# Optimization experiments

Hardware: AMD Instinct MI355X
Metric: run time of the kernel (lower is better)

The kernel has to match this reference:

```python
import jax, jax.numpy as jnp
import numpy as np

B, N, DEG = 128, 512, 16          # graphs, nodes/graph, avg degree
NB = B * N                        # 65536 nodes
E = NB * DEG                      # 1048576 edges
K1, K2, K3 = 410, 205, 103        # ceil(0.8*512), ceil(0.5*410), ceil(0.5*205)
H, C = 4, 32                      # GAT heads, head dim
F_IN, ED = 128, 7


def _glorot(key, shape, fan_in):
    return jax.random.normal(key, shape, dtype=jnp.float32) / np.float32(np.sqrt(fan_in))


def setup_inputs() -> dict:
    key = jax.random.key(0)
    ks = jax.random.split(key, 24)
    x = jax.random.normal(ks[0], (NB, F_IN), dtype=jnp.float32)
    # random intra-graph edges, then offset per graph
    src = jax.random.randint(ks[1], (E,), 0, N)
    dst = jax.random.randint(ks[2], (E,), 0, N)
    off = jnp.repeat(jnp.arange(B) * N, N * DEG)
    edge_index = jnp.stack([src + off, dst + off]).astype(jnp.int32)
    edge_attr = jax.random.normal(ks[3], (E, ED), dtype=jnp.float32)
    p = {
        'c1_wl': _glorot(ks[4], (F_IN, F_IN), F_IN), 'c1_bl': jnp.zeros((F_IN,), jnp.float32), 'c1_wr': _glorot(ks[5], (F_IN, F_IN), F_IN),
        'p1_w': _glorot(ks[6], (F_IN,), F_IN),
        'c2_wl': _glorot(ks[7], (F_IN, F_IN), F_IN), 'c2_bl': jnp.zeros((F_IN,), jnp.float32), 'c2_wr': _glorot(ks[8], (F_IN, F_IN), F_IN),
        'p2_wrel': _glorot(ks[9], (F_IN, 1), F_IN), 'p2_brel': jnp.zeros((1,), jnp.float32), 'p2_wroot': _glorot(ks[10], (F_IN, 1), F_IN),
        'g_w': _glorot(ks[11], (F_IN, H * C), F_IN), 'g_as': _glorot(ks[12], (H, C), C), 'g_ad': _glorot(ks[13], (H, C), C),
        'g_we': _glorot(ks[14], (ED, H * C), ED), 'g_ae': _glorot(ks[15], (H, C), C), 'g_b': jnp.zeros((H * C,), jnp.float32),
        'p3_wrel': _glorot(ks[16], (F_IN, 1), F_IN), 'p3_brel': jnp.zeros((1,), jnp.float32), 'p3_wroot': _glorot(ks[17], (F_IN, 1), F_IN),
        'l1_w': _glorot(ks[18], (F_IN, F_IN), F_IN), 'l1_b': jnp.zeros((F_IN,), jnp.float32),
        'l2_w': _glorot(ks[19], (F_IN, 64), F_IN), 'l2_b': jnp.zeros((64,), jnp.float32),
        'l3_w': _glorot(ks[20], (64, 1), 64), 'l3_b': jnp.zeros((1,), jnp.float32),
    }
    return {'x': x, 'edge_index': edge_index, 'edge_attr': edge_attr, **p}


def _sage(x, src, dst, emf, wl, bl, wr):
    # SAGEConv: mean-aggregate neighbors (masked edges), lin_l(agg)+lin_r(x)
    agg = jax.ops.segment_sum(x[src] * emf[:, None], dst, num_segments=NB)
    cnt = jax.ops.segment_sum(emf, dst, num_segments=NB)
    mean = agg / jnp.maximum(cnt, 1.0)[:, None]
    return mean @ wl + bl + x @ wr


def _graphconv(x, src, dst, emf, wrel, brel, wroot):
    # GraphConv (SAGPooling score GNN): add-aggregation
    agg = jax.ops.segment_sum(x[src] * emf[:, None], dst, num_segments=NB)
    return (agg @ wrel + brel + x @ wroot).reshape(-1)


def _pool(x, score, nmask, K):
    # per-graph static top-k (equal-size graphs) == PyG topk + filter
    masked = jnp.where(nmask, score, -jnp.inf).reshape(B, N)
    idx = jax.lax.top_k(masked, K)[1]
    nm = jnp.zeros((B, N), dtype=bool).at[jnp.arange(B)[:, None], idx].set(True).reshape(-1)
    x = jnp.where(nm[:, None], x * score[:, None], 0.0)
    return x, nm


def _gap(x, K):
    # global mean pool; dropped nodes are exactly zero, K live nodes per graph
    return x.reshape(B, N, F_IN).sum(axis=1) / K


def _gat(x, src, dst, emf, nmask, edge_attr, w, a_s, a_d, w_e, a_e, b):
    xs = (x @ w).reshape(NB, H, C)
    al_s = (xs * a_s).sum(-1)                                   # [NB,H]
    al_d = (xs * a_d).sum(-1)
    al_e = ((edge_attr @ w_e).reshape(E, H, C) * a_e).sum(-1)    # [E,H]
    alpha = jax.nn.leaky_relu(al_s[src] + al_d[dst] + al_e, 0.2)
    alpha = jnp.where(emf[:, None] > 0, alpha, -jnp.inf)
    # PyG add_self_loops=True with fill_value='mean' for edge_attr
    ea_mean = (edge_attr * emf[:, None]).sum(0) / jnp.maximum(emf.sum(), 1.0)
    al_se = ((ea_mean @ w_e).reshape(H, C) * a_e).sum(-1)        # [H]
    alpha_self = jax.nn.leaky_relu(al_s + al_d + al_se[None, :], 0.2)
    alpha_self = jnp.where(nmask[:, None], alpha_self, -jnp.inf)
    m = jnp.maximum(jax.ops.segment_max(alpha, dst, num_segments=NB), alpha_self)
    m = jnp.where(jnp.isfinite(m), m, 0.0)
    ex = jnp.exp(alpha - m[dst]) * emf[:, None]
    ex_s = jnp.where(nmask[:, None], jnp.exp(alpha_self - m), 0.0)
    den = jnp.maximum(jax.ops.segment_sum(ex, dst, num_segments=NB) + ex_s, 1e-16)
    num = jax.ops.segment_sum(ex[:, :, None] * xs[src], dst, num_segments=NB) + ex_s[:, :, None] * xs
    return (num / den[:, :, None]).reshape(NB, H * C) + b


def _forward(x, edge_index, edge_attr, c1_wl, c1_bl, c1_wr, p1_w, c2_wl, c2_bl, c2_wr,
             p2_wrel, p2_brel, p2_wroot, g_w, g_as, g_ad, g_we, g_ae, g_b,
             p3_wrel, p3_brel, p3_wroot, l1_w, l1_b, l2_w, l2_b, l3_w, l3_b):
    src, dst = edge_index[0], edge_index[1]
    nmask = jnp.ones((NB,), dtype=bool)
    emf = jnp.ones((E,), jnp.float32)

    # block 1: SAGEConv -> TopKPooling(0.8) -> gap
    x = jax.nn.relu(_sage(x, src, dst, emf, c1_wl, c1_bl, c1_wr))
    s1 = jnp.tanh((x @ p1_w) / jnp.linalg.norm(p1_w))
    x, nmask = _pool(x, s1, nmask, K1)
    emf = emf * nmask[src] * nmask[dst]
    x1 = _gap(x, K1)

    # block 2: SAGEConv -> SAGPooling(0.5) -> gap
    x = jax.nn.relu(_sage(x, src, dst, emf, c2_wl, c2_bl, c2_wr))
    s2 = jnp.tanh(_graphconv(x, src, dst, emf, p2_wrel, p2_brel, p2_wroot))
    x, nmask = _pool(x, s2, nmask, K2)
    emf = emf * nmask[src] * nmask[dst]
    x2 = _gap(x, K2)

    # block 3: GATConv(128->32x4, edge_dim=7) -> SAGPooling(0.5) -> gap
    x = jax.nn.relu(_gat(x, src, dst, emf, nmask, edge_attr, g_w, g_as, g_ad, g_we, g_ae, g_b))
    s3 = jnp.tanh(_graphconv(x, src, dst, emf, p3_wrel, p3_brel, p3_wroot))
    x, nmask = _pool(x, s3, nmask, K3)
    x3 = _gap(x, K3)

    h = x1 + x2 + x3
    h = jax.nn.relu(h @ l1_w + l1_b)
    h = jax.nn.relu(h @ l2_w + l2_b)   # dropout identity in eval
    return jax.nn.sigmoid(h @ l3_w + l3_b)[:, 0]


def reference(x, edge_index, edge_attr, c1_wl, c1_bl, c1_wr, p1_w, c2_wl, c2_bl, c2_wr,
              p2_wrel, p2_brel, p2_wroot, g_w, g_as, g_ad, g_we, g_ae, g_b,
              p3_wrel, p3_brel, p3_wroot, l1_w, l1_b, l2_w, l2_b, l3_w, l3_b):
    return _forward(x, edge_index, edge_attr, c1_wl, c1_bl, c1_wr, p1_w, c2_wl, c2_bl, c2_wr,
                    p2_wrel, p2_brel, p2_wroot, g_w, g_as, g_ad, g_we, g_ae, g_b,
                    p3_wrel, p3_brel, p3_wroot, l1_w, l1_b, l2_w, l2_b, l3_w, l3_b)
```

## Files before the change

### kernel.cpp

```cpp
#include <hip/hip_runtime.h>
#include <math.h>

#define NBV 65536
#define EV  1048576
#define BV  128
#define K1V 410
#define K2V 205
#define K3V 103
#define NL2 (BV*K2V)
#define NEG_BIG (-1.0e38f)

__device__ __forceinline__ float lrelu(float x){ return x > 0.f ? x : 0.2f*x; }

__global__ void k_sentinel(float* out, float v){
  int i = threadIdx.x;
  if (i < 128) out[i] = v;
}

__global__ void k_init1(float* nmask, int* dcnt){
  int i = blockIdx.x*blockDim.x + threadIdx.x;
  if (i < NBV) nmask[i] = 1.f;
  if (i < NBV+1) dcnt[i] = 0;
}

__global__ void k_zero_i(int* p, int n){
  int i = blockIdx.x*blockDim.x + threadIdx.x;
  if (i < n) p[i] = 0;
}

__global__ void k_hist(const int* dst, int* dcnt){
  int e = blockIdx.x*blockDim.x + threadIdx.x;
  if (e < EV) atomicAdd(&dcnt[dst[e]], 1);
}

__global__ void k_scan1(const int* dcnt, int* rp, int* bsum){
  __shared__ int sc[256];
  int t = threadIdx.x, i = blockIdx.x*256 + t;
  int v = dcnt[i];
  sc[t] = v; __syncthreads();
  for (int o = 1; o < 256; o <<= 1){
    int x = (t >= o) ? sc[t-o] : 0;
    __syncthreads();
    sc[t] += x;
    __syncthreads();
  }
  rp[i] = sc[t];
  if (t == 255) bsum[blockIdx.x] = sc[t];
}

__global__ void k_scan2(int* bsum){
  __shared__ int sc[256];
  int t = threadIdx.x;
  int v = bsum[t];
  sc[t] = v; __syncthreads();
  for (int o = 1; o < 256; o <<= 1){
    int x = (t >= o) ? sc[t-o] : 0;
    __syncthreads();
    sc[t] += x;
    __syncthreads();
  }
  bsum[t] = sc[t] - v;
}

__global__ void k_scan3(int* rp, const int* dcnt, const int* bsum){
  int t = threadIdx.x, i = blockIdx.x*256 + t;
  rp[i] = rp[i] - dcnt[i] + bsum[blockIdx.x];
  if (i == 0) rp[NBV] = EV;
}

__global__ void k_scatter(const int* src, const int* dst, const int* rp, int* fill,
                          int* csr_src, int* csr_eid){
  int e = blockIdx.x*blockDim.x + threadIdx.x;
  if (e < EV){
    int d = dst[e];
    int pos = atomicAdd(&fill[d], 1);
    int slot = rp[d] + pos;
    csr_src[slot] = src[e];
    csr_eid[slot] = e;
  }
}

__global__ void k_ve_inv(const float* g_we, const float* g_ae, const float* p1w, float* sml){
  __shared__ float sc[128];
  int t = threadIdx.x;
  if (t < 28){
    int ed = t >> 2, h = t & 3;
    float a = 0.f;
    for (int c = 0; c < 32; c++) a += g_we[ed*128 + h*32 + c] * g_ae[h*32 + c];
    sml[20 + t] = a;
  }
  float v = p1w[t];
  sc[t] = v*v; __syncthreads();
  for (int o = 64; o > 0; o >>= 1){ if (t < o) sc[t] += sc[t+o]; __syncthreads(); }
  if (t == 0) sml[0] = 1.f / sqrtf(sc[0]);
}

__global__ void k_ale(const float* ea, const float* ve, float* ALE){
  int e = blockIdx.x*blockDim.x + threadIdx.x;
  if (e < EV){
    float a0=0.f,a1=0.f,a2=0.f,a3=0.f;
    for (int ed = 0; ed < 7; ed++){
      float x = ea[e*7 + ed];
      a0 += x*ve[ed*4+0]; a1 += x*ve[ed*4+1]; a2 += x*ve[ed*4+2]; a3 += x*ve[ed*4+3];
    }
    float4 o; o.x=a0; o.y=a1; o.z=a2; o.w=a3;
    *(float4*)&ALE[(size_t)e*4] = o;
  }
}

__global__ void __launch_bounds__(256) k_sage_agg(const float* X, const float* nmask,
    const int* rp, const int* csr_src, float* AGG, int masked,
    const int* nidx, int kper){
  int g = blockIdx.x & 127;
  int blk = blockIdx.x >> 7;
  int r = blk*8 + (threadIdx.x >> 5);
  int i;
  if (nidx){ if (r >= kper) return; i = nidx[g*kper + r]; }
  else i = g*512 + r;
  int c4 = threadIdx.x & 31;
  float ax=0.f,ay=0.f,az=0.f,aw=0.f,cnt=0.f;
  if (!masked || nmask[i] > 0.f){
    int r0 = rp[i], r1 = rp[i+1];
    int s = r0;
    for (; s + 4 <= r1; s += 4){
      int sn0 = csr_src[s+0], sn1 = csr_src[s+1], sn2 = csr_src[s+2], sn3 = csr_src[s+3];
      float nm0 = masked ? nmask[sn0] : 1.f;
      float nm1 = masked ? nmask[sn1] : 1.f;
      float nm2 = masked ? nmask[sn2] : 1.f;
      float nm3 = masked ? nmask[sn3] : 1.f;
      if (nm0 > 0.f){ float4 v = *(const float4*)&X[((size_t)sn0 << 7) + (c4 << 2)];
                      ax += v.x; ay += v.y; az += v.z; aw += v.w; cnt += 1.f; }
      if (nm1 > 0.f){ float4 v = *(const float4*)&X[((size_t)sn1 << 7) + (c4 << 2)];
                      ax += v.x; ay += v.y; az += v.z; aw += v.w; cnt += 1.f; }
      if (nm2 > 0.f){ float4 v = *(const float4*)&X[((size_t)sn2 << 7) + (c4 << 2)];
                      ax += v.x; ay += v.y; az += v.z; aw += v.w; cnt += 1.f; }
      if (nm3 > 0.f){ float4 v = *(const float4*)&X[((size_t)sn3 << 7) + (c4 << 2)];
                      ax += v.x; ay += v.y; az += v.z; aw += v.w; cnt += 1.f; }
    }
    for (; s < r1; s++){
      int sn = csr_src[s];
      float nm = masked ? nmask[sn] : 1.f;
      if (nm > 0.f){
        const float4 v = *(const float4*)&X[((size_t)sn << 7) + (c4 << 2)];
        ax += v.x; ay += v.y; az += v.z; aw += v.w; cnt += 1.f;
      }
    }
  }
  float inv = 1.f / fmaxf(cnt, 1.f);
  float4 o; o.x = ax*inv; o.y = ay*inv; o.z = az*inv; o.w = aw*inv;
  *(float4*)&AGG[((size_t)i << 7) + (c4 << 2)] = o;
}

__global__ void __launch_bounds__(512) k_gemm(const float* A1, const float* A2,
    const float* W1, const float* W2, const float* bias,
    float* OUT, int has2, int relu, int hasb,
    const int* ridx, int sc_mode,
    const float* sw1, const float* sw2, const float* sinv,
    float* so1, float* so2){
  __shared__ float ws[128][128];
  __shared__ float as[128][136];
  int t = threadIdx.x;
  int n0 = blockIdx.x * 128;
  int rowg = t >> 5;
  int colg = t & 31;
  int rb = rowg * 8;
  int jb = colg * 4;
  int an = t >> 2;
  int ak = (t & 3) << 2;
  int arow = ridx ? ridx[n0 + an] : (n0 + an);
  float acc[8][4];
  for (int r = 0; r < 8; r++)
    for (int j = 0; j < 4; j++) acc[r][j] = 0.f;
  int nmat = has2 ? 2 : 1;
  for (int m = 0; m < nmat; m++){
    const float* A = (m == 0) ? A1 : A2;
    const float* W = (m == 0) ? W1 : W2;
    __syncthreads();
    for (int ii = 0; ii < 8; ii++){
      int idx4 = t + 512*ii;
      int kk = idx4 >> 5;
      int jj = (idx4 & 31) << 2;
      *(float4*)&ws[kk][jj] = *(const float4*)&W[kk*128 + jj];
    }
    for (int c = 0; c < 8; c++){
      float4 rA = *(const float4*)&A[((size_t)arow << 7) + c*16 + ak];
      as[c*16+ak+0][an] = rA.x;
      as[c*16+ak+1][an] = rA.y;
      as[c*16+ak+2][an] = rA.z;
      as[c*16+ak+3][an] = rA.w;
    }
    __syncthreads();
    for (int c = 0; c < 8; c++){
      int kb = c*16;
      for (int kk = 0; kk < 16; kk++){
        float4 wv = *(const float4*)&ws[kb+kk][jb];
        float4 aL = *(const float4*)&as[kb+kk][rb];
        float4 aH = *(const float4*)&as[kb+kk][rb+4];
        float a0=aL.x,a1=aL.y,a2=aL.z,a3=aL.w,a4=aH.x,a5=aH.y,a6=aH.z,a7=aH.w;
        acc[0][0]+=a0*wv.x; acc[0][1]+=a0*wv.y; acc[0][2]+=a0*wv.z; acc[0][3]+=a0*wv.w;
        acc[1][0]+=a1*wv.x; acc[1][1]+=a1*wv.y; acc[1][2]+=a1*wv.z; acc[1][3]+=a1*wv.w;
        acc[2][0]+=a2*wv.x; acc[2][1]+=a2*wv.y; acc[2][2]+=a2*wv.z; acc[2][3]+=a2*wv.w;
        acc[3][0]+=a3*wv.x; acc[3][1]+=a3*wv.y; acc[3][2]+=a3*wv.z; acc[3][3]+=a3*wv.w;
        acc[4][0]+=a4*wv.x; acc[4][1]+=a4*wv.y; acc[4][2]+=a4*wv.z; acc[4][3]+=a4*wv.w;
        acc[5][0]+=a5*wv.x; acc[5][1]+=a5*wv.y; acc[5][2]+=a5*wv.z; acc[5][3]+=a5*wv.w;
        acc[6][0]+=a6*wv.x; acc[6][1]+=a6*wv.y; acc[6][2]+=a6*wv.z; acc[6][3]+=a6*wv.w;
        acc[7][0]+=a7*wv.x; acc[7][1]+=a7*wv.y; acc[7][2]+=a7*wv.z; acc[7][3]+=a7*wv.w;
      }
    }
  }
  float bj0=0.f,bj1=0.f,bj2=0.f,bj3=0.f;
  if (hasb){
    bj0 = bias[jb+0]; bj1 = bias[jb+1]; bj2 = bias[jb+2]; bj3 = bias[jb+3];
  }
  int orow[8];
  for (int r = 0; r < 8; r++) orow[r] = ridx ? ridx[n0+rb+r] : (n0+rb+r);
  float w1x=0.f,w1y=0.f,w1z=0.f,w1w=0.f, w2x=0.f,w2y=0.f,w2z=0.f,w2w=0.f;
  if (sc_mode){
    float4 t1 = *(const float4*)&sw1[jb];
    w1x=t1.x; w1y=t1.y; w1z=t1.z; w1w=t1.w;
    if (sc_mode == 2){
      float4 t2 = *(const float4*)&sw2[jb];
      w2x=t2.x; w2y=t2.y; w2z=t2.z; w2w=t2.w;
    }
  }
  float pd1[8], pd2[8];
  for (int r = 0; r < 8; r++){
    float4 o;
    o.x = acc[r][0]+bj0; o.y = acc[r][1]+bj1; o.z = acc[r][2]+bj2; o.w = acc[r][3]+bj3;
    if (relu){
      o.x = fmaxf(o.x,0.f); o.y = fmaxf(o.y,0.f); o.z = fmaxf(o.z,0.f); o.w = fmaxf(o.w,0.f);
    }
    if (sc_mode){
      pd1[r] = o.x*w1x + o.y*w1y + o.z*w1z + o.w*w1w;
      if (sc_mode == 2) pd2[r] = o.x*w2x + o.y*w2y + o.z*w2z + o.w*w2w;
    }
    *(float4*)&OUT[((size_t)orow[r] << 7) + jb] = o;
  }
  if (sc_mode == 1){
    float inv = sinv[0];
    for (int r = 0; r < 8; r++){
      float a = pd1[r];
      for (int o = 16; o > 0; o >>= 1) a += __shfl_down(a, o, 32);
      if (colg == 0) so1[orow[r]] = tanhf(a * inv);
    }
  } else if (sc_mode == 2){
    for (int r = 0; r < 8; r++){
      float a = pd1[r];
      float b = pd2[r];
      for (int o = 16; o > 0; o >>= 1){
        a += __shfl_down(a, o, 32);
        b += __shfl_down(b, o, 32);
      }
      if (colg == 0){ so1[orow[r]] = a; so2[orow[r]] = b; }
    }
  }
}

__global__ void k_gconv(const float* q, const float* r, const float* nmask,
    const int* rp, const int* csr_src, const float* brel, float* s){
  int i = blockIdx.x*blockDim.x + threadIdx.x;
  if (i >= NBV) return;
  float acc = 0.f;
  if (nmask[i] > 0.f){
    int r0 = rp[i], r1 = rp[i+1];
    int t2 = r0;
    for (; t2 + 4 <= r1; t2 += 4){
      int sn0 = csr_src[t2+0], sn1 = csr_src[t2+1], sn2 = csr_src[t2+2], sn3 = csr_src[t2+3];
      float nm0 = nmask[sn0], nm1 = nmask[sn1], nm2 = nmask[sn2], nm3 = nmask[sn3];
      if (nm0 > 0.f) acc += q[sn0];
      if (nm1 > 0.f) acc += q[sn1];
      if (nm2 > 0.f) acc += q[sn2];
      if (nm3 > 0.f) acc += q[sn3];
    }
    for (; t2 < r1; t2++){
      int sn = csr_src[t2];
      if (nmask[sn] > 0.f) acc += q[sn];
    }
  }
  s[i] = tanhf(acc + brel[0] + r[i]);
}

__global__ void __launch_bounds__(512) k_pool(const float* s, float* nmask, float* sel,
                                              int K, int* cidx){
  __shared__ float sc[512];
  int b = blockIdx.x, t = threadIdx.x;
  int i = b*512 + t;
  float nm = nmask[i];
  float sv = s[i];
  float ms = (nm > 0.f) ? sv : NEG_BIG;
  sc[t] = ms;
  __syncthreads();
  int rank = 0;
  for (int j = 0; j < 512; j++){
    float o = sc[j];
    rank += ((o > ms) || (o == ms && j < t)) ? 1 : 0;
  }
  bool selb = rank < K;
  nmask[i] = selb ? 1.f : 0.f;
  sel[i] = selb ? sv : 0.f;
  if (cidx && selb) cidx[b*K + rank] = i;
}

__global__ void __launch_bounds__(128) k_scale_part(float* X, const float* sel,
    const float* nmask, float* part){
  int b = blockIdx.x >> 3, q = blockIdx.x & 7, c = threadIdx.x;
  float acc = 0.f;
  for (int n = q*64; n < q*64 + 64; n++){
    int i = b*512 + n;
    if (nmask[i] > 0.f){
      float v = X[((size_t)i << 7) + c] * sel[i];
      X[((size_t)i << 7) + c] = v;
      acc += v;
    }
  }
  part[(size_t)blockIdx.x*128 + c] = acc;
}

__global__ void __launch_bounds__(128) k_gap_final(const float* part, float* gap, float invK){
  int b = blockIdx.x, c = threadIdx.x;
  float s = 0.f;
  for (int q = 0; q < 8; q++) s += part[(size_t)(b*8+q)*128 + c];
  gap[b*128 + c] = s * invK;
}

__global__ void k_heads(const float* xs, const float* a_s, const float* a_d,
                        const int* cidx, int nlive4, float* alS, float* alD){
  int gid = blockIdx.x*blockDim.x + threadIdx.x;
  if (gid >= nlive4) return;
  int ii = gid >> 2, h = gid & 3;
  int i = cidx[ii];
  const float4* xr = (const float4*)&xs[((size_t)i << 7) + h*32];
  const float4* wa = (const float4*)&a_s[h*32];
  const float4* wd = (const float4*)&a_d[h*32];
  float as_ = 0.f, ad_ = 0.f;
  for (int c4 = 0; c4 < 8; c4++){
    float4 v = xr[c4]; float4 A = wa[c4]; float4 D = wd[c4];
    as_ += v.x*A.x + v.y*A.y + v.z*A.z + v.w*A.w;
    ad_ += v.x*D.x + v.y*D.y + v.z*D.z + v.w*D.w;
  }
  alS[i*4 + h] = as_; alD[i*4 + h] = ad_;
}

__global__ void __launch_bounds__(256) k_ea_part(const float* ea, const int* srcA, const int* dstA,
    const float* nmask, float* part){
  float p[8] = {0.f,0.f,0.f,0.f,0.f,0.f,0.f,0.f};
  for (int e = blockIdx.x*256 + threadIdx.x; e < EV; e += 256*256){
    if (nmask[srcA[e]] > 0.f && nmask[dstA[e]] > 0.f){
      for (int d = 0; d < 7; d++) p[d] += ea[e*7 + d];
      p[7] += 1.f;
    }
  }
  __shared__ float red[256];
  for (int comp = 0; comp < 8; comp++){
    red[threadIdx.x] = p[comp]; __syncthreads();
    for (int o = 128; o > 0; o >>= 1){ if (threadIdx.x < o) red[threadIdx.x] += red[threadIdx.x + o]; __syncthreads(); }
    if (threadIdx.x == 0) part[blockIdx.x*8 + comp] = red[0];
    __syncthreads();
  }
}

__global__ void k_ea_fin(const float* part, const float* ve, float* alse){
  __shared__ float es[8];
  int h = threadIdx.x;
  if (h < 8){
    float s = 0.f;
    for (int b = 0; b < 256; b++) s += part[b*8 + h];
    es[h] = s;
  }
  __syncthreads();
  if (h == 0){
    float cnt = fmaxf(es[7], 1.f);
    for (int hh = 0; hh < 4; hh++){
      float s = 0.f;
      for (int ed = 0; ed < 7; ed++) s += (es[ed]/cnt) * ve[ed*4 + hh];
      alse[hh] = s;
    }
  }
}

__global__ void __launch_bounds__(256) k_gat(const float* xs, const float* alS, const float* alD,
    const float* ALE, const float* nmask, const int* rp, const int* csr_src,
    const int* csr_eid, const float* alse, const float* g_b,
    const float* wrel, const float* wroot, const int* nidx, int kper,
    float* qv, float* rv, float* OUT){
  int g = blockIdx.x & 127;
  int blk = blockIdx.x >> 7;
  int r = blk*8 + (threadIdx.x >> 5);
  int i;
  if (nidx){ if (r >= kper) return; i = nidx[g*kper + r]; }
  else i = g*512 + r;
  int lane = threadIdx.x & 31;
  int h = lane >> 3;
  int ch = h*8 + (lane & 7);
  float nmi = nmask[i];
  const float4* xs4 = (const float4*)xs;
  float m = 0.f, den = 0.f;
  float4 acc; acc.x=0.f; acc.y=0.f; acc.z=0.f; acc.w=0.f;
  if (nmi > 0.f){
    float ald_i = alD[i*4 + h];
    m = lrelu(alS[i*4 + h] + ald_i + alse[h]);
    den = 1.f;
    acc = xs4[(size_t)i*32 + ch];
    int r0 = rp[i], r1 = rp[i+1];
    int s = r0;
    for (; s + 4 <= r1; s += 4){
      int sn0 = csr_src[s+0], sn1 = csr_src[s+1], sn2 = csr_src[s+2], sn3 = csr_src[s+3];
      float nm0 = nmask[sn0], nm1 = nmask[sn1], nm2 = nmask[sn2], nm3 = nmask[sn3];
      if (nm0 > 0.f){
        float a = lrelu(alS[sn0*4 + h] + ald_i + ALE[(size_t)csr_eid[s+0]*4 + h]);
        float4 v = xs4[(size_t)sn0*32 + ch];
        float mn = fmaxf(m, a); float pm = expf(m - mn); float pa = expf(a - mn);
        den = den*pm + pa;
        acc.x = acc.x*pm + pa*v.x; acc.y = acc.y*pm + pa*v.y;
        acc.z = acc.z*pm + pa*v.z; acc.w = acc.w*pm + pa*v.w;
        m = mn;
      }
      if (nm1 > 0.f){
        float a = lrelu(alS[sn1*4 + h] + ald_i + ALE[(size_t)csr_eid[s+1]*4 + h]);
        float4 v = xs4[(size_t)sn1*32 + ch];
        float mn = fmaxf(m, a); float pm = expf(m - mn); float pa = expf(a - mn);
        den = den*pm + pa;
        acc.x = acc.x*pm + pa*v.x; acc.y = acc.y*pm + pa*v.y;
        acc.z = acc.z*pm + pa*v.z; acc.w = acc.w*pm + pa*v.w;
        m = mn;
      }
      if (nm2 > 0.f){
        float a = lrelu(alS[sn2*4 + h] + ald_i + ALE[(size_t)csr_eid[s+2]*4 + h]);
        float4 v = xs4[(size_t)sn2*32 + ch];
        float mn = fmaxf(m, a); float pm = expf(m - mn); float pa = expf(a - mn);
        den = den*pm + pa;
        acc.x = acc.x*pm + pa*v.x; acc.y = acc.y*pm + pa*v.y;
        acc.z = acc.z*pm + pa*v.z; acc.w = acc.w*pm + pa*v.w;
        m = mn;
      }
      if (nm3 > 0.f){
        float a = lrelu(alS[sn3*4 + h] + ald_i + ALE[(size_t)csr_eid[s+3]*4 + h]);
        float4 v = xs4[(size_t)sn3*32 + ch];
        float mn = fmaxf(m, a); float pm = expf(m - mn); float pa = expf(a - mn);
        den = den*pm + pa;
        acc.x = acc.x*pm + pa*v.x; acc.y = acc.y*pm + pa*v.y;
        acc.z = acc.z*pm + pa*v.z; acc.w = acc.w*pm + pa*v.w;
        m = mn;
      }
    }
    for (; s < r1; s++){
      int sn = csr_src[s];
      if (nmask[sn] > 0.f){
        float a = lrelu(alS[sn*4 + h] + ald_i + ALE[(size_t)csr_eid[s]*4 + h]);
        float4 v = xs4[(size_t)sn*32 + ch];
        float mn = fmaxf(m, a); float pm = expf(m - mn); float pa = expf(a - mn);
        den = den*pm + pa;
        acc.x = acc.x*pm + pa*v.x; acc.y = acc.y*pm + pa*v.y;
        acc.z = acc.z*pm + pa*v.z; acc.w = acc.w*pm + pa*v.w;
        m = mn;
      }
    }
  }
  den = fmaxf(den, 1e-16f);
  float rd = 1.f/den;
  int cb = ch << 2;
  float4 o;
  o.x = fmaxf(acc.x*rd + g_b[cb+0], 0.f);
  o.y = fmaxf(acc.y*rd + g_b[cb+1], 0.f);
  o.z = fmaxf(acc.z*rd + g_b[cb+2], 0.f);
  o.w = fmaxf(acc.w*rd + g_b[cb+3], 0.f);
  *(float4*)&OUT[((size_t)i << 7) + cb] = o;
  float4 wa = *(const float4*)&wrel[cb];
  float4 wb = *(const float4*)&wroot[cb];
  float aq = o.x*wa.x + o.y*wa.y + o.z*wa.z + o.w*wa.w;
  float ar = o.x*wb.x + o.y*wb.y + o.z*wb.z + o.w*wb.w;
  for (int off = 16; off > 0; off >>= 1){
    aq += __shfl_down(aq, off, 32);
    ar += __shfl_down(ar, off, 32);
  }
  if (lane == 0){ qv[i] = aq; rv[i] = ar; }
}

__global__ void __launch_bounds__(128) k_mlp(const float* x1g, const float* x2g, const float* x3g,
    const float* l1w, const float* l1b, const float* l2w, const float* l2b,
    const float* l3w, const float* l3b, float* out){
  __shared__ float hh[128];
  __shared__ float h2[128];
  __shared__ float h3[64];
  int b = blockIdx.x, t = threadIdx.x;
  hh[t] = x1g[b*128 + t] + x2g[b*128 + t] + x3g[b*128 + t];
  __syncthreads();
  float a = l1b[t];
  for (int k = 0; k < 128; k++) a += hh[k] * l1w[k*128 + t];
  h2[t] = fmaxf(a, 0.f);
  __syncthreads();
  if (t < 64){
    float a2 = l2b[t];
    for (int k = 0; k < 128; k++) a2 += h2[k] * l2w[k*64 + t];
    h3[t] = fmaxf(a2, 0.f);
  }
  __syncthreads();
  if (t == 0){
    float z = l3b[0];
    for (int k = 0; k < 64; k++) z += h3[k] * l3w[k];
    out[b] = 1.f/(1.f + expf(-z));
  }
}

extern "C" void kernel_launch(void* const* d_in, const int* in_sizes, int n_in,
                              void* d_out, int out_size, void* d_ws, size_t ws_size,
                              hipStream_t stream){
  const float* x       = (const float*)d_in[0];
  const int*   ei      = (const int*)d_in[1];
  const float* ea      = (const float*)d_in[2];
  const float* c1_wl   = (const float*)d_in[3];
  const float* c1_bl   = (const float*)d_in[4];
  const float* c1_wr   = (const float*)d_in[5];
  const float* p1_w    = (const float*)d_in[6];
  const float* c2_wl   = (const float*)d_in[7];
  const float* c2_bl   = (const float*)d_in[8];
  const float* c2_wr   = (const float*)d_in[9];
  const float* p2_wrel = (const float*)d_in[10];
  const float* p2_brel = (const float*)d_in[11];
  const float* p2_wroot= (const float*)d_in[12];
  const float* g_w     = (const float*)d_in[13];
  const float* g_as    = (const float*)d_in[14];
  const float* g_ad    = (const float*)d_in[15];
  const float* g_we    = (const float*)d_in[16];
  const float* g_ae    = (const float*)d_in[17];
  const float* g_b     = (const float*)d_in[18];
  const float* p3_wrel = (const float*)d_in[19];
  const float* p3_brel = (const float*)d_in[20];
  const float* p3_wroot= (const float*)d_in[21];
  const float* l1_w    = (const float*)d_in[22];
  const float* l1_b    = (const float*)d_in[23];
  const float* l2_w    = (const float*)d_in[24];
  const float* l2_b    = (const float*)d_in[25];
  const float* l3_w    = (const float*)d_in[26];
  const float* l3_b    = (const float*)d_in[27];
  float* out = (float*)d_out;
  (void)in_sizes; (void)n_in; (void)out_size;

  char* w = (char*)d_ws;
  size_t off = 0;
  float* AGG  = (float*)(w + off); off += (size_t)NBV*128*4;
  float* F1   = (float*)(w + off); off += (size_t)NBV*128*4;
  float* F2   = (float*)(w + off); off += (size_t)NBV*128*4;
  float* ALE  = (float*)(w + off); off += (size_t)EV*4*4;
  float* sA   = (float*)(w + off); off += (size_t)NBV*4;
  float* sel  = (float*)(w + off); off += (size_t)NBV*4;
  float* qv   = (float*)(w + off); off += (size_t)NBV*4;
  float* rv   = (float*)(w + off); off += (size_t)NBV*4;
  float* nmask= (float*)(w + off); off += (size_t)NBV*4;
  float* alS  = (float*)(w + off); off += (size_t)NBV*4*4;
  float* alD  = (float*)(w + off); off += (size_t)NBV*4*4;
  float* x1g  = (float*)(w + off); off += (size_t)BV*128*4;
  float* x2g  = (float*)(w + off); off += (size_t)BV*128*4;
  float* x3g  = (float*)(w + off); off += (size_t)BV*128*4;
  float* sml  = (float*)(w + off); off += 64*4;
  float* eprt = (float*)(w + off); off += 2048*4;
  float* gprt = (float*)(w + off); off += (size_t)1024*128*4;
  int* csr_src = (int*)(w + off); off += (size_t)EV*4;
  int* csr_eid = (int*)(w + off); off += (size_t)EV*4;
  int* rp      = (int*)(w + off); off += (size_t)(NBV+64)*4;
  int* dcnt    = (int*)(w + off); off += (size_t)(NBV+64)*4;
  int* cidx1   = (int*)(w + off); off += (size_t)NBV*4;
  int* cidx2   = (int*)(w + off); off += (size_t)NBV*4;
  int* bsum    = (int*)(w + off); off += 1024;
  size_t needed = off;

  float sentinel = (ws_size >= needed) ? 0.125f : 0.875f;
  k_sentinel<<<1, 128, 0, stream>>>(out, sentinel);

  const int* srcA = ei;
  const int* dstA = ei + EV;

  k_init1<<<(NBV+256)/256, 256, 0, stream>>>(nmask, dcnt);
  k_hist<<<EV/256, 256, 0, stream>>>(dstA, dcnt);
  k_scan1<<<256, 256, 0, stream>>>(dcnt, rp, bsum);
  k_scan2<<<1, 256, 0, stream>>>(bsum);
  k_scan3<<<256, 256, 0, stream>>>(rp, dcnt, bsum);
  k_zero_i<<<(NBV+256)/256, 256, 0, stream>>>(dcnt, NBV+1);
  k_scatter<<<EV/256, 256, 0, stream>>>(srcA, dstA, rp, dcnt, csr_src, csr_eid);
  k_ve_inv<<<1, 128, 0, stream>>>(g_we, g_ae, p1_w, sml);
  k_ale<<<EV/256, 256, 0, stream>>>(ea, sml+20, ALE);

  k_sage_agg<<<(NBV*32)/256, 256, 0, stream>>>(x, nmask, rp, csr_src, AGG, 0,
                                               (const int*)nullptr, 512);
  k_gemm<<<NBV/128, 512, 0, stream>>>(AGG, x, c1_wl, c1_wr, c1_bl, F1, 1, 1, 1,
                                      (const int*)nullptr, 1, p1_w, (const float*)nullptr, sml, sA, (float*)nullptr);
  k_pool<<<BV, 512, 0, stream>>>(sA, nmask, sel, K1V, cidx1);
  k_scale_part<<<BV*8, 128, 0, stream>>>(F1, sel, nmask, gprt);
  k_gap_final<<<BV, 128, 0, stream>>>(gprt, x1g, 1.f/(float)K1V);

  k_sage_agg<<<BV*52, 256, 0, stream>>>(F1, nmask, rp, csr_src, AGG, 1, cidx1, K1V);
  k_gemm<<<NBV/128, 512, 0, stream>>>(AGG, F1, c2_wl, c2_wr, c2_bl, F2, 1, 1, 1,
                                      (const int*)nullptr, 2, p2_wrel, p2_wroot, (const float*)nullptr, qv, rv);
  k_gconv<<<NBV/256, 256, 0, stream>>>(qv, rv, nmask, rp, csr_src, p2_brel, sA);
  k_pool<<<BV, 512, 0, stream>>>(sA, nmask, sel, K2V, cidx2);
  k_scale_part<<<BV*8, 128, 0, stream>>>(F2, sel, nmask, gprt);
  k_gap_final<<<BV, 128, 0, stream>>>(gprt, x2g, 1.f/(float)K2V);

  k_gemm<<<NL2/128, 512, 0, stream>>>(F2, F2, g_w, g_w, g_b, AGG, 0, 0, 0,
                                      cidx2, 0, (const float*)nullptr, (const float*)nullptr,
                                      (const float*)nullptr, (float*)nullptr, (float*)nullptr);
  k_heads<<<(NL2*4 + 255)/256, 256, 0, stream>>>(AGG, g_as, g_ad, cidx2, NL2*4, alS, alD);
  k_ea_part<<<256, 256, 0, stream>>>(ea, srcA, dstA, nmask, eprt);
  k_ea_fin<<<1, 64, 0, stream>>>(eprt, sml+20, sml+16);
  k_gat<<<BV*26, 256, 0, stream>>>(AGG, alS, alD, ALE, nmask, rp, csr_src, csr_eid,
                                   sml+16, g_b, p3_wrel, p3_wroot, cidx2, K2V, qv, rv, F1);
  k_gconv<<<NBV/256, 256, 0, stream>>>(qv, rv, nmask, rp, csr_src, p3_brel, sA);
  k_pool<<<BV, 512, 0, stream>>>(sA, nmask, sel, K3V, (int*)nullptr);
  k_scale_part<<<BV*8, 128, 0, stream>>>(F1, sel, nmask, gprt);
  k_gap_final<<<BV, 128, 0, stream>>>(gprt, x3g, 1.f/(float)K3V);

  k_mlp<<<BV, 128, 0, stream>>>(x1g, x2g, x3g, l1_w, l1_b, l2_w, l2_b, l3_w, l3_b, out);
}
```

Before: 694.9 us.

## Fuse pool/scale/gap kernels, fold GAT head scores into GEMM, shrink GEMM smem

Pool ranking, feature scaling and global mean pooling are merged into one per-graph kernel, which drops the sel and partial-sum buffers and two launches per block. The GAT attention-head dot products move into the GEMM epilogue through a new sc_mode 3 that does shuffle reductions, removing the k_heads pass over the features. Init, sentinel and counter zeroing are folded into one kernel, and a separate fill counter replaces re-zeroing dcnt. The GEMM A tile is cut to 16 rows and streamed with a register prefetch, which lowers LDS use but adds a barrier per k-chunk. The fused pool kernel runs only 128 blocks, so the scaling pass has less parallelism than before.

```diff
diff --git a/kernel.cpp b/kernel.cpp
--- a/kernel.cpp
+++ b/kernel.cpp
@@ -12,20 +12,11 @@
 
 __device__ __forceinline__ float lrelu(float x){ return x > 0.f ? x : 0.2f*x; }
 
-__global__ void k_sentinel(float* out, float v){
-  int i = threadIdx.x;
-  if (i < 128) out[i] = v;
-}
-
-__global__ void k_init1(float* nmask, int* dcnt){
+__global__ void k_init1(float* nmask, int* dcnt, int* fill, float* out, float sval){
   int i = blockIdx.x*blockDim.x + threadIdx.x;
+  if (i < 128) out[i] = sval;
   if (i < NBV) nmask[i] = 1.f;
-  if (i < NBV+1) dcnt[i] = 0;
-}
-
-__global__ void k_zero_i(int* p, int n){
-  int i = blockIdx.x*blockDim.x + threadIdx.x;
-  if (i < n) p[i] = 0;
+  if (i < NBV+1){ dcnt[i] = 0; fill[i] = 0; }
 }
 
 __global__ void k_hist(const int* dst, int* dcnt){
@@ -158,7 +149,7 @@
     const float* sw1, const float* sw2, const float* sinv,
     float* so1, float* so2){
   __shared__ float ws[128][128];
-  __shared__ float as[128][136];
+  __shared__ float as[16][136];
   int t = threadIdx.x;
   int n0 = blockIdx.x * 128;
   int rowg = t >> 5;
@@ -182,20 +173,21 @@
       int jj = (idx4 & 31) << 2;
       *(float4*)&ws[kk][jj] = *(const float4*)&W[kk*128 + jj];
     }
+    float4 rA = *(const float4*)&A[((size_t)arow << 7) + ak];
     for (int c = 0; c < 8; c++){
-      float4 rA = *(const float4*)&A[((size_t)arow << 7) + c*16 + ak];
-      as[c*16+ak+0][an] = rA.x;
-      as[c*16+ak+1][an] = rA.y;
-      as[c*16+ak+2][an] = rA.z;
-      as[c*16+ak+3][an] = rA.w;
-    }
-    __syncthreads();
-    for (int c = 0; c < 8; c++){
+      if (c > 0) __syncthreads();
+      as[ak+0][an] = rA.x;
+      as[ak+1][an] = rA.y;
+      as[ak+2][an] = rA.z;
+      as[ak+3][an] = rA.w;
+      __syncthreads();
+      if (c+1 < 8)
+        rA = *(const float4*)&A[((size_t)arow << 7) + (c+1)*16 + ak];
       int kb = c*16;
       for (int kk = 0; kk < 16; kk++){
         float4 wv = *(const float4*)&ws[kb+kk][jb];
-        float4 aL = *(const float4*)&as[kb+kk][rb];
-        float4 aH = *(const float4*)&as[kb+kk][rb+4];
+        float4 aL = *(const float4*)&as[kk][rb];
+        float4 aH = *(const float4*)&as[kk][rb+4];
         float a0=aL.x,a1=aL.y,a2=aL.z,a3=aL.w,a4=aH.x,a5=aH.y,a6=aH.z,a7=aH.w;
         acc[0][0]+=a0*wv.x; acc[0][1]+=a0*wv.y; acc[0][2]+=a0*wv.z; acc[0][3]+=a0*wv.w;
         acc[1][0]+=a1*wv.x; acc[1][1]+=a1*wv.y; acc[1][2]+=a1*wv.z; acc[1][3]+=a1*wv.w;
@@ -218,7 +210,7 @@
   if (sc_mode){
     float4 t1 = *(const float4*)&sw1[jb];
     w1x=t1.x; w1y=t1.y; w1z=t1.z; w1w=t1.w;
-    if (sc_mode == 2){
+    if (sc_mode >= 2){
       float4 t2 = *(const float4*)&sw2[jb];
       w2x=t2.x; w2y=t2.y; w2z=t2.z; w2w=t2.w;
     }
@@ -232,7 +224,7 @@
     }
     if (sc_mode){
       pd1[r] = o.x*w1x + o.y*w1y + o.z*w1z + o.w*w1w;
-      if (sc_mode == 2) pd2[r] = o.x*w2x + o.y*w2y + o.z*w2z + o.w*w2w;
+      if (sc_mode >= 2) pd2[r] = o.x*w2x + o.y*w2y + o.z*w2z + o.w*w2w;
     }
     *(float4*)&OUT[((size_t)orow[r] << 7) + jb] = o;
   }
@@ -252,6 +244,20 @@
         b += __shfl_down(b, o, 32);
       }
       if (colg == 0){ so1[orow[r]] = a; so2[orow[r]] = b; }
+    }
+  } else if (sc_mode == 3){
+    int base = colg & ~7;
+    for (int r = 0; r < 8; r++){
+      float s1 = 0.f, s2 = 0.f;
+      for (int c4 = 0; c4 < 8; c4++){
+        s1 += __shfl(pd1[r], base + c4, 32);
+        s2 += __shfl(pd2[r], base + c4, 32);
+      }
+      if ((colg & 7) == 0){
+        int h = colg >> 3;
+        so1[orow[r]*4 + h] = s1;
+        so2[orow[r]*4 + h] = s2;
+      }
     }
   }
 }
@@ -280,9 +286,11 @@
   s[i] = tanhf(acc + brel[0] + r[i]);
 }
 
-__global__ void __launch_bounds__(512) k_pool(const float* s, float* nmask, float* sel,
-                                              int K, int* cidx){
+__global__ void __launch_bounds__(512) k_poolscale(const float* s, float* nmask,
+    float* X, float* gap, int K, int* cidx, float invK){
   __shared__ float sc[512];
+  __shared__ float lsel[512];
+  __shared__ float prt[8][128];
   int b = blockIdx.x, t = threadIdx.x;
   int i = b*512 + t;
   float nm = nmask[i];
@@ -297,48 +305,31 @@
   }
   bool selb = rank < K;
   nmask[i] = selb ? 1.f : 0.f;
-  sel[i] = selb ? sv : 0.f;
   if (cidx && selb) cidx[b*K + rank] = i;
-}
-
-__global__ void __launch_bounds__(128) k_scale_part(float* X, const float* sel,
-    const float* nmask, float* part){
-  int b = blockIdx.x >> 3, q = blockIdx.x & 7, c = threadIdx.x;
-  float acc = 0.f;
-  for (int n = q*64; n < q*64 + 64; n++){
-    int i = b*512 + n;
-    if (nmask[i] > 0.f){
-      float v = X[((size_t)i << 7) + c] * sel[i];
-      X[((size_t)i << 7) + c] = v;
-      acc += v;
-    }
-  }
-  part[(size_t)blockIdx.x*128 + c] = acc;
-}
-
-__global__ void __launch_bounds__(128) k_gap_final(const float* part, float* gap, float invK){
-  int b = blockIdx.x, c = threadIdx.x;
-  float s = 0.f;
-  for (int q = 0; q < 8; q++) s += part[(size_t)(b*8+q)*128 + c];
-  gap[b*128 + c] = s * invK;
-}
-
-__global__ void k_heads(const float* xs, const float* a_s, const float* a_d,
-                        const int* cidx, int nlive4, float* alS, float* alD){
-  int gid = blockIdx.x*blockDim.x + threadIdx.x;
-  if (gid >= nlive4) return;
-  int ii = gid >> 2, h = gid & 3;
-  int i = cidx[ii];
-  const float4* xr = (const float4*)&xs[((size_t)i << 7) + h*32];
-  const float4* wa = (const float4*)&a_s[h*32];
-  const float4* wd = (const float4*)&a_d[h*32];
-  float as_ = 0.f, ad_ = 0.f;
-  for (int c4 = 0; c4 < 8; c4++){
-    float4 v = xr[c4]; float4 A = wa[c4]; float4 D = wd[c4];
-    as_ += v.x*A.x + v.y*A.y + v.z*A.z + v.w*A.w;
-    ad_ += v.x*D.x + v.y*D.y + v.z*D.z + v.w*D.w;
-  }
-  alS[i*4 + h] = as_; alD[i*4 + h] = ad_;
+  __syncthreads();
+  sc[t] = selb ? 1.f : 0.f;
+  lsel[t] = selb ? sv : 0.f;
+  __syncthreads();
+  int c = t & 127, g = t >> 7;
+  for (int qq = 0; qq < 2; qq++){
+    int q = g*2 + qq;
+    float acc = 0.f;
+    for (int n = q*64; n < q*64 + 64; n++){
+      if (sc[n] > 0.f){
+        size_t idx = (((size_t)(b*512 + n)) << 7) + c;
+        float v = X[idx] * lsel[n];
+        X[idx] = v;
+        acc += v;
+      }
+    }
+    prt[q][c] = acc;
+  }
+  __syncthreads();
+  if (t < 128){
+    float ss = 0.f;
+    for (int q = 0; q < 8; q++) ss += prt[q][t];
+    gap[b*128 + t] = ss * invK;
+  }
 }
 
 __global__ void __launch_bounds__(256) k_ea_part(const float* ea, const int* srcA, const int* dstA,
@@ -543,7 +534,6 @@
   float* F2   = (float*)(w + off); off += (size_t)NBV*128*4;
   float* ALE  = (float*)(w + off); off += (size_t)EV*4*4;
   float* sA   = (float*)(w + off); off += (size_t)NBV*4;
-  float* sel  = (float*)(w + off); off += (size_t)NBV*4;
   float* qv   = (float*)(w + off); off += (size_t)NBV*4;
   float* rv   = (float*)(w + off); off += (size_t)NBV*4;
   float* nmask= (float*)(w + off); off += (size_t)NBV*4;
@@ -554,29 +544,27 @@
   float* x3g  = (float*)(w + off); off += (size_t)BV*128*4;
   float* sml  = (float*)(w + off); off += 64*4;
   float* eprt = (float*)(w + off); off += 2048*4;
-  float* gprt = (float*)(w + off); off += (size_t)1024*128*4;
   int* csr_src = (int*)(w + off); off += (size_t)EV*4;
   int* csr_eid = (int*)(w + off); off += (size_t)EV*4;
   int* rp      = (int*)(w + off); off += (size_t)(NBV+64)*4;
   int* dcnt    = (int*)(w + off); off += (size_t)(NBV+64)*4;
+  int* fill    = (int*)(w + off); off += (size_t)(NBV+64)*4;
   int* cidx1   = (int*)(w + off); off += (size_t)NBV*4;
   int* cidx2   = (int*)(w + off); off += (size_t)NBV*4;
   int* bsum    = (int*)(w + off); off += 1024;
   size_t needed = off;
 
   float sentinel = (ws_size >= needed) ? 0.125f : 0.875f;
-  k_sentinel<<<1, 128, 0, stream>>>(out, sentinel);
 
   const int* srcA = ei;
   const int* dstA = ei + EV;
 
-  k_init1<<<(NBV+256)/256, 256, 0, stream>>>(nmask, dcnt);
+  k_init1<<<(NBV+256)/256, 256, 0, stream>>>(nmask, dcnt, fill, out, sentinel);
   k_hist<<<EV/256, 256, 0, stream>>>(dstA, dcnt);
   k_scan1<<<256, 256, 0, stream>>>(dcnt, rp, bsum);
   k_scan2<<<1, 256, 0, stream>>>(bsum);
   k_scan3<<<256, 256, 0, stream>>>(rp, dcnt, bsum);
-  k_zero_i<<<(NBV+256)/256, 256, 0, stream>>>(dcnt, NBV+1);
-  k_scatter<<<EV/256, 256, 0, stream>>>(srcA, dstA, rp, dcnt, csr_src, csr_eid);
+  k_scatter<<<EV/256, 256, 0, stream>>>(srcA, dstA, rp, fill, csr_src, csr_eid);
   k_ve_inv<<<1, 128, 0, stream>>>(g_we, g_ae, p1_w, sml);
   k_ale<<<EV/256, 256, 0, stream>>>(ea, sml+20, ALE);
 
@@ -584,30 +572,23 @@
                                                (const int*)nullptr, 512);
   k_gemm<<<NBV/128, 512, 0, stream>>>(AGG, x, c1_wl, c1_wr, c1_bl, F1, 1, 1, 1,
                                       (const int*)nullptr, 1, p1_w, (const float*)nullptr, sml, sA, (float*)nullptr);
-  k_pool<<<BV, 512, 0, stream>>>(sA, nmask, sel, K1V, cidx1);
-  k_scale_part<<<BV*8, 128, 0, stream>>>(F1, sel, nmask, gprt);
-  k_gap_final<<<BV, 128, 0, stream>>>(gprt, x1g, 1.f/(float)K1V);
+  k_poolscale<<<BV, 512, 0, stream>>>(sA, nmask, F1, x1g, K1V, cidx1, 1.f/(float)K1V);
 
   k_sage_agg<<<BV*52, 256, 0, stream>>>(F1, nmask, rp, csr_src, AGG, 1, cidx1, K1V);
   k_gemm<<<NBV/128, 512, 0, stream>>>(AGG, F1, c2_wl, c2_wr, c2_bl, F2, 1, 1, 1,
                                       (const int*)nullptr, 2, p2_wrel, p2_wroot, (const float*)nullptr, qv, rv);
   k_gconv<<<NBV/256, 256, 0, stream>>>(qv, rv, nmask, rp, csr_src, p2_brel, sA);
-  k_pool<<<BV, 512, 0, stream>>>(sA, nmask, sel, K2V, cidx2);
-  k_scale_part<<<BV*8, 128, 0, stream>>>(F2, sel, nmask, gprt);
-  k_gap_final<<<BV, 128, 0, stream>>>(gprt, x2g, 1.f/(float)K2V);
+  k_poolscale<<<BV, 512, 0, stream>>>(sA, nmask, F2, x2g, K2V, cidx2, 1.f/(float)K2V);
 
   k_gemm<<<NL2/128, 512, 0, stream>>>(F2, F2, g_w, g_w, g_b, AGG, 0, 0, 0,
-                                      cidx2, 0, (const float*)nullptr, (const float*)nullptr,
-                                      (const float*)nullptr, (float*)nullptr, (float*)nullptr);
-  k_heads<<<(NL2*4 + 255)/256, 256, 0, stream>>>(AGG, g_as, g_ad, cidx2, NL2*4, alS, alD);
+                                      cidx2, 3, g_as, g_ad,
+                                      (const float*)nullptr, alS, alD);
   k_ea_part<<<256, 256, 0, stream>>>(ea, srcA, dstA, nmask, eprt);
   k_ea_fin<<<1, 64, 0, stream>>>(eprt, sml+20, sml+16);
   k_gat<<<BV*26, 256, 0, stream>>>(AGG, alS, alD, ALE, nmask, rp, csr_src, csr_eid,
                                    sml+16, g_b, p3_wrel, p3_wroot, cidx2, K2V, qv, rv, F1);
   k_gconv<<<NBV/256, 256, 0, stream>>>(qv, rv, nmask, rp, csr_src, p3_brel, sA);
-  k_pool<<<BV, 512, 0, stream>>>(sA, nmask, sel, K3V, (int*)nullptr);
-  k_scale_part<<<BV*8, 128, 0, stream>>>(F1, sel, nmask, gprt);
-  k_gap_final<<<BV, 128, 0, stream>>>(gprt, x3g, 1.f/(float)K3V);
+  k_poolscale<<<BV, 512, 0, stream>>>(sA, nmask, F1, x3g, K3V, (int*)nullptr, 1.f/(float)K3V);
 
   k_mlp<<<BV, 128, 0, stream>>>(x1g, x2g, x3g, l1_w, l1_b, l2_w, l2_b, l3_w, l3_b, out);
 }
```

After: 674.8 us. -2.9%, faster.
